# Performance work log

Hardware: AMD Instinct MI355X
Metric: run time of the kernel (lower is better)

The kernel has to match this reference:

```python
import jax, jax.numpy as jnp
import numpy as np

B, L, D, H, FF = 2, 4096, 512, 8, 2048
HD = D // H
EPS = 1e-5


def _layer_norm(x, g, b):
    mu = jnp.mean(x, axis=-1, keepdims=True)
    var = jnp.mean(jnp.square(x - mu), axis=-1, keepdims=True)
    return (x - mu) * jax.lax.rsqrt(var + EPS) * g + b


def setup_inputs() -> dict:
    key = jax.random.key(0)
    ks = jax.random.split(key, 16)
    s = 1.0 / np.sqrt(D)
    inp = {
        'x': jax.random.normal(ks[0], (B, L, D), dtype=jnp.float32),
        'Wq': jax.random.normal(ks[1], (D, D), dtype=jnp.float32) * s,
        'bq': jnp.zeros((D,), jnp.float32),
        'Wk': jax.random.normal(ks[2], (D, D), dtype=jnp.float32) * s,
        'bk': jnp.zeros((D,), jnp.float32),
        'Wv': jax.random.normal(ks[3], (D, D), dtype=jnp.float32) * s,
        'bv': jnp.zeros((D,), jnp.float32),
        'Wo': jax.random.normal(ks[4], (D, D), dtype=jnp.float32) * s,
        'bo': jnp.zeros((D,), jnp.float32),
        'ln1_g': jnp.ones((D,), jnp.float32),
        'ln1_b': jnp.zeros((D,), jnp.float32),
        'W1': jax.random.normal(ks[5], (D, FF), dtype=jnp.float32) * s,
        'b1': jnp.zeros((FF,), jnp.float32),
        'W2': jax.random.normal(ks[6], (FF, D), dtype=jnp.float32) * (1.0 / np.sqrt(FF)),
        'b2': jnp.zeros((D,), jnp.float32),
        'ln2_g': jnp.ones((D,), jnp.float32),
        'ln2_b': jnp.zeros((D,), jnp.float32),
        'window': 128,
    }
    return inp


def reference(x, Wq, bq, Wk, bk, Wv, bv, Wo, bo, ln1_g, ln1_b, W1, b1, W2, b2, ln2_g, ln2_b, window):
    # ---- local (banded) self-attention, matching nn.MultiheadAttention math ----
    q = (x @ Wq + bq).reshape(B, L, H, HD)
    k = (x @ Wk + bk).reshape(B, L, H, HD)
    v = (x @ Wv + bv).reshape(B, L, H, HD)
    scale = 1.0 / np.sqrt(HD)
    scores = jnp.einsum('bqhd,bkhd->bhqk', q, k) * scale  # [B,H,L,L]
    idx = jnp.arange(L)
    band = jnp.abs(idx[None, :] - idx[:, None]) > window   # True = masked
    scores = jnp.where(band[None, None], -jnp.inf, scores)
    probs = jax.nn.softmax(scores, axis=-1)
    attn = jnp.einsum('bhqk,bkhd->bqhd', probs, v).reshape(B, L, D)
    attn = attn @ Wo + bo
    # ---- residual + norm1 ----
    h = _layer_norm(x + attn, ln1_g, ln1_b)
    # ---- FFN + residual + norm2 (dropout=0 at eval) ----
    ff = jax.nn.relu(h @ W1 + b1) @ W2 + b2
    return _layer_norm(h + ff, ln2_g, ln2_b)
```

## Files before the change

### kernel.cpp

```cpp
#include <hip/hip_runtime.h>

namespace {

constexpr int B = 2, L = 4096, D = 512, H = 8, FF = 2048;
constexpr int M = B * L;
constexpr float LN_EPS = 1e-5f;

typedef __attribute__((ext_vector_type(8))) short short8;
typedef __attribute__((ext_vector_type(4))) float floatx4;

typedef __attribute__((address_space(3))) unsigned int lds_uint;
typedef const __attribute__((address_space(1))) unsigned int glob_uint;

__device__ __forceinline__ void gl_lds16(const unsigned short* g, unsigned short* l) {
  __builtin_amdgcn_global_load_lds((glob_uint*)g, (lds_uint*)l, 16, 0, 0);
}

__device__ __forceinline__ unsigned short f2bf(float f) {
  union { float f; unsigned u; } v; v.f = f;
  unsigned r = v.u + 0x7FFFu + ((v.u >> 16) & 1u);
  return (unsigned short)(r >> 16);
}

__device__ __forceinline__ float bf2f(unsigned short b) {
  union { unsigned u; float f; } v; v.u = ((unsigned)b) << 16;
  return v.f;
}

__global__ __launch_bounds__(256)
void k_prep(const float* __restrict__ x,
            const float* __restrict__ Wq, const float* __restrict__ Wk,
            const float* __restrict__ Wv, const float* __restrict__ Wo,
            const float* __restrict__ W1, const float* __restrict__ W2,
            const float* __restrict__ bq, const float* __restrict__ bk,
            const float* __restrict__ bv,
            unsigned short* __restrict__ Xb,
            unsigned short* __restrict__ WqkvT, unsigned short* __restrict__ WoT,
            unsigned short* __restrict__ W1T, unsigned short* __restrict__ W2T,
            float* __restrict__ bqkv) {
  __shared__ unsigned short tile[64 * 72];
  if (blockIdx.x < 4102) {
    int tid = blockIdx.x * blockDim.x + threadIdx.x;
    if (tid < 1048576) {
      float4 v = ((const float4*)x)[tid];
      ((ushort4*)Xb)[tid] = make_ushort4(f2bf(v.x), f2bf(v.y), f2bf(v.z), f2bf(v.w));
      return;
    }
    int u = tid - 1048576;
    if (u < 1536) bqkv[u] = (u < 512) ? bq[u] : (u < 1024 ? bk[u - 512] : bv[u - 1024]);
    return;
  }
  const int t = blockIdx.x - 4102;
  const float* src; unsigned short* dst; int Ns, Kd, n0, k0, nsrc0;
  if (t < 192) {
    int nt = t % 24, kt = t / 24; int ng = nt * 64;
    src = ng < 512 ? Wq : (ng < 1024 ? Wk : Wv);
    Ns = 512; Kd = 512; n0 = ng; nsrc0 = ng & 511; k0 = kt * 64; dst = WqkvT;
  } else if (t < 256) {
    int u = t - 192; int nt = u % 8, kt = u / 8;
    src = Wo; Ns = 512; Kd = 512; n0 = nt * 64; nsrc0 = n0; k0 = kt * 64; dst = WoT;
  } else if (t < 512) {
    int u = t - 256; int nt = u % 32, kt = u / 32;
    src = W1; Ns = 2048; Kd = 512; n0 = nt * 64; nsrc0 = n0; k0 = kt * 64; dst = W1T;
  } else {
    int u = t - 512; int nt = u % 8, kt = u / 8;
    src = W2; Ns = 512; Kd = 2048; n0 = nt * 64; nsrc0 = n0; k0 = kt * 64; dst = W2T;
  }
  const int tid = threadIdx.x;
  {
    int r = tid >> 2, cs = (tid & 3) * 16;
    const float4* sp = (const float4*)(src + (size_t)(k0 + r) * Ns + nsrc0 + cs);
    unsigned short* tp = &tile[r * 72 + cs];
#pragma unroll
    for (int i = 0; i < 4; ++i) {
      float4 v = sp[i];
      tp[i * 4 + 0] = f2bf(v.x); tp[i * 4 + 1] = f2bf(v.y);
      tp[i * 4 + 2] = f2bf(v.z); tp[i * 4 + 3] = f2bf(v.w);
    }
  }
  __syncthreads();
  {
    int n = tid >> 2, ks = (tid & 3) * 16;
    unsigned short buf[16];
#pragma unroll
    for (int e = 0; e < 16; ++e) buf[e] = tile[(ks + e) * 72 + n];
    unsigned short* dp = dst + (size_t)(n0 + n) * Kd + k0 + ks;
    *(short8*)dp = *(const short8*)&buf[0];
    *(short8*)(dp + 8) = *(const short8*)&buf[8];
  }
}

template <int EPI>
__global__ __launch_bounds__(256, 3)
void k_gemm(const unsigned short* __restrict__ A, const unsigned short* __restrict__ BT,
            const float* __restrict__ bias, void* __restrict__ Cout,
            unsigned short* __restrict__ Vout,
            const int klen, const int N) {
  __shared__ unsigned short lA[2][128 * 32];
  __shared__ unsigned short lB[2][128 * 32];
  const int tid = threadIdx.x;
  const int wave = tid >> 6, lane = tid & 63;
  const int quad = lane >> 4, l16 = lane & 15;
  const int m0 = blockIdx.y * 128, n0 = blockIdx.x * 128;
  const int wm = (wave >> 1) * 64, wn = (wave & 1) * 64;
  const int kbeg = blockIdx.z * klen;
  const size_t Kdim = (size_t)klen * gridDim.z;

  const floatx4 fzero = {0.f, 0.f, 0.f, 0.f};
  floatx4 acc[4][4];
#pragma unroll
  for (int i = 0; i < 4; ++i)
#pragma unroll
    for (int j = 0; j < 4; ++j) acc[i][j] = fzero;

  const int r0 = tid >> 2, o0 = (tid & 3) * 8;
  const int r1 = (256 + tid) >> 2, o1 = (tid & 3) * 8;
  const unsigned short* Ag0 = A + (size_t)(m0 + r0) * Kdim + kbeg + o0;
  const unsigned short* Ag1 = A + (size_t)(m0 + r1) * Kdim + kbeg + o1;
  const unsigned short* Bg0 = BT + (size_t)(n0 + r0) * Kdim + kbeg + o0;
  const unsigned short* Bg1 = BT + (size_t)(n0 + r1) * Kdim + kbeg + o1;

  auto stage = [&](int buf, int kt) {
    gl_lds16(Ag0 + kt, &lA[buf][wave * 512]);
    gl_lds16(Ag1 + kt, &lA[buf][(4 + wave) * 512]);
    gl_lds16(Bg0 + kt, &lB[buf][wave * 512]);
    gl_lds16(Bg1 + kt, &lB[buf][(4 + wave) * 512]);
  };

  stage(0, 0);
  __syncthreads();

  int buf = 0;
  for (int kt = 0; kt < klen; kt += 32, buf ^= 1) {
    if (kt + 32 < klen) stage(buf ^ 1, kt + 32);
    short8 af[4], bf[4];
#pragma unroll
    for (int i = 0; i < 4; ++i)
      af[i] = *(const short8*)&lA[buf][(wm + i * 16 + l16) * 32 + quad * 8];
#pragma unroll
    for (int j = 0; j < 4; ++j)
      bf[j] = *(const short8*)&lB[buf][(wn + j * 16 + l16) * 32 + quad * 8];
#pragma unroll
    for (int i = 0; i < 4; ++i)
#pragma unroll
      for (int j = 0; j < 4; ++j)
        acc[i][j] = __builtin_amdgcn_mfma_f32_16x16x32_bf16(af[i], bf[j], acc[i][j], 0, 0, 0);
    __syncthreads();
  }

  float* outf = (float*)Cout + (size_t)blockIdx.z * M * N;
  const bool vblock = (EPI == 3) && (n0 >= 1024);
#pragma unroll
  for (int j = 0; j < 4; ++j) {
    const int col = n0 + wn + j * 16 + l16;
    const float bv = (blockIdx.z == 0) ? bias[col] : 0.f;
#pragma unroll
    for (int i = 0; i < 4; ++i) {
      const int row = m0 + wm + i * 16 + quad * 4;
      if (EPI == 3 && vblock) {
        const int hh = (col - 1024) >> 6, dd = (col - 1024) & 63;
        const int bb = row >> 12, keyl = row & 4095;
        ushort4 pk = make_ushort4(f2bf(acc[i][j][0] + bv), f2bf(acc[i][j][1] + bv),
                                  f2bf(acc[i][j][2] + bv), f2bf(acc[i][j][3] + bv));
        *(ushort4*)(Vout + ((size_t)(bb * 8 + hh) * 64 + dd) * L + keyl) = pk;
      } else {
#pragma unroll
        for (int r = 0; r < 4; ++r) {
          float v = acc[i][j][r] + bv;
          if (EPI == 1) v = fmaxf(v, 0.f);
          if (EPI == 2)
            outf[(size_t)(row + r) * N + col] = v;
          else
            ((unsigned short*)Cout)[(size_t)(row + r) * N + col] = f2bf(v);
        }
      }
    }
  }
}

__global__ __launch_bounds__(256, 3)
void k_attn(const unsigned short* __restrict__ QKV, const unsigned short* __restrict__ Vg,
            unsigned short* __restrict__ attnb, const int* __restrict__ wptr) {
  const int W = wptr[0];
  __shared__ unsigned short Kt[2][4096];
  __shared__ unsigned short Vt[2][4096];
  __shared__ unsigned short Pb[4][16 * 72];
  const int tid = threadIdx.x;
  const int wave = tid >> 6, lane = tid & 63;
  const int quad = lane >> 4, l16 = lane & 15;
  const int blk = blockIdx.x;
  const int qt = blk & 63, h = (blk >> 6) & 7, b = blk >> 9;
  const int q0blk = qt * 64;
  const int q0 = q0blk + wave * 16;
  const float scale = 0.125f;

  const unsigned short* Kbase = QKV + (size_t)(b * L) * 1536 + 512 + h * 64;
  const unsigned short* Vh = Vg + (size_t)(b * 8 + h) * 64 * L;

  auto stage = [&](int buf, int jbg) {
#pragma unroll
    for (int i = 0; i < 2; ++i) {
      int c = i * 256 + tid;
      int key = jbg + (c >> 3);
      int keyc = key < 0 ? 0 : (key > L - 1 ? L - 1 : key);
      int dpart = (c & 7) ^ ((c >> 3) & 7);
      gl_lds16(Kbase + (size_t)keyc * 1536 + dpart * 8,
               &Kt[buf][(i * 256 + wave * 64) * 8]);
    }
#pragma unroll
    for (int i = 0; i < 2; ++i) {
      int c = i * 256 + tid;
      int d = c >> 3;
      int kpart = (c & 7) ^ (d & 7);
      int kb = jbg + kpart * 8;
      kb = kb < 0 ? 0 : (kb > L - 8 ? L - 8 : kb);
      gl_lds16(Vh + (size_t)d * L + kb,
               &Vt[buf][(i * 256 + wave * 64) * 8]);
    }
  };

  const unsigned short* Qp = QKV + (size_t)(b * L + q0 + l16) * 1536 + h * 64;
  short8 qf0 = *(const short8*)(Qp + quad * 8);
  short8 qf1 = *(const short8*)(Qp + 32 + quad * 8);

  const floatx4 fzero = {0.f, 0.f, 0.f, 0.f};
  floatx4 o[4];
#pragma unroll
  for (int i = 0; i < 4; ++i) o[i] = fzero;
  float lsum[4] = {0.f, 0.f, 0.f, 0.f};
  unsigned short* lp = Pb[wave];
  const int sw = l16 & 7;

  stage(0, q0blk - 128);
  __syncthreads();

  for (int it = 0; it < 5; ++it) {
    const int jbg = q0blk - 128 + it * 64;
    if (it < 4) stage((it + 1) & 1, jbg + 64);
    const unsigned short* lk = Kt[it & 1];
    const unsigned short* lv = Vt[it & 1];
    floatx4 s[4];
#pragma unroll
    for (int ct = 0; ct < 4; ++ct) {
      int key = ct * 16 + l16;
      const short8 kf0 = *(const short8*)&lk[(key * 8 + (quad ^ sw)) * 8];
      const short8 kf1 = *(const short8*)&lk[(key * 8 + ((quad + 4) ^ sw)) * 8];
      floatx4 z = fzero;
      z = __builtin_amdgcn_mfma_f32_16x16x32_bf16(qf0, kf0, z, 0, 0, 0);
      z = __builtin_amdgcn_mfma_f32_16x16x32_bf16(qf1, kf1, z, 0, 0, 0);
      s[ct] = z;
    }
#pragma unroll
    for (int r = 0; r < 4; ++r) {
      int q = q0 + quad * 4 + r;
#pragma unroll
      for (int ct = 0; ct < 4; ++ct) {
        int key = jbg + ct * 16 + l16;
        int d = q - key; d = d < 0 ? -d : d;
        bool ok = (key >= 0) && (key < L) && (d <= W);
        float p = ok ? __expf(s[ct][r] * scale) : 0.f;
        lsum[r] += p;
        lp[(quad * 4 + r) * 72 + ct * 16 + l16] = f2bf(p);
      }
    }
    short8 pf0 = *(const short8*)&lp[l16 * 72 + quad * 8];
    short8 pf1 = *(const short8*)&lp[l16 * 72 + 32 + quad * 8];
#pragma unroll
    for (int nt = 0; nt < 4; ++nt) {
      int d = nt * 16 + l16;
      const short8 vf0 = *(const short8*)&lv[(d * 8 + (quad ^ sw)) * 8];
      const short8 vf1 = *(const short8*)&lv[(d * 8 + ((quad + 4) ^ sw)) * 8];
      o[nt] = __builtin_amdgcn_mfma_f32_16x16x32_bf16(pf0, vf0, o[nt], 0, 0, 0);
      o[nt] = __builtin_amdgcn_mfma_f32_16x16x32_bf16(pf1, vf1, o[nt], 0, 0, 0);
    }
    __syncthreads();
  }
#pragma unroll
  for (int r = 0; r < 4; ++r) {
#pragma unroll
    for (int dd = 1; dd < 16; dd <<= 1) lsum[r] += __shfl_xor(lsum[r], dd, 64);
  }
#pragma unroll
  for (int r = 0; r < 4; ++r) {
    float inv = 1.f / lsum[r];
    size_t base = (size_t)(b * L + q0 + quad * 4 + r) * 512 + h * 64;
#pragma unroll
    for (int nt = 0; nt < 4; ++nt)
      attnb[base + nt * 16 + l16] = f2bf(o[nt][r] * inv);
  }
}

template <int RESBF>
__global__ __launch_bounds__(256, 2)
void k_res_ln(const float* __restrict__ t0, const float* __restrict__ t1,
              const void* __restrict__ res,
              const float* __restrict__ gamma, const float* __restrict__ beta,
              float* __restrict__ outf, unsigned short* __restrict__ outb) {
  const int wave = threadIdx.x >> 6, lane = threadIdx.x & 63;
  const int row = blockIdx.x * 4 + wave;
  const float4* tv = (const float4*)(t0 + (size_t)row * D);
  float4 a0 = tv[lane], a1 = tv[lane + 64];
  float4 b0, b1;
  if (RESBF) {
    const ushort4* rv = (const ushort4*)((const unsigned short*)res + (size_t)row * D);
    ushort4 u0 = rv[lane], u1 = rv[lane + 64];
    b0 = make_float4(bf2f(u0.x), bf2f(u0.y), bf2f(u0.z), bf2f(u0.w));
    b1 = make_float4(bf2f(u1.x), bf2f(u1.y), bf2f(u1.z), bf2f(u1.w));
  } else {
    const float4* rv = (const float4*)((const float*)res + (size_t)row * D);
    b0 = rv[lane]; b1 = rv[lane + 64];
  }
  float4 y0 = make_float4(a0.x + b0.x, a0.y + b0.y, a0.z + b0.z, a0.w + b0.w);
  float4 y1 = make_float4(a1.x + b1.x, a1.y + b1.y, a1.z + b1.z, a1.w + b1.w);
  {
    const float4* uv = (const float4*)(t1 + (size_t)row * D);
    float4 c0 = uv[lane], c1 = uv[lane + 64];
    y0.x += c0.x; y0.y += c0.y; y0.z += c0.z; y0.w += c0.w;
    y1.x += c1.x; y1.y += c1.y; y1.z += c1.z; y1.w += c1.w;
  }
  float s = y0.x + y0.y + y0.z + y0.w + y1.x + y1.y + y1.z + y1.w;
  float q = y0.x * y0.x + y0.y * y0.y + y0.z * y0.z + y0.w * y0.w +
            y1.x * y1.x + y1.y * y1.y + y1.z * y1.z + y1.w * y1.w;
#pragma unroll
  for (int d = 1; d < 64; d <<= 1) {
    s += __shfl_xor(s, d, 64);
    q += __shfl_xor(q, d, 64);
  }
  const float mean = s * (1.f / D);
  const float var = q * (1.f / D) - mean * mean;
  const float rstd = rsqrtf(var + LN_EPS);
  float4 g0 = ((const float4*)gamma)[lane], g1 = ((const float4*)gamma)[lane + 64];
  float4 e0 = ((const float4*)beta)[lane], e1 = ((const float4*)beta)[lane + 64];
  float4 o0 = make_float4((y0.x - mean) * rstd * g0.x + e0.x, (y0.y - mean) * rstd * g0.y + e0.y,
                          (y0.z - mean) * rstd * g0.z + e0.z, (y0.w - mean) * rstd * g0.w + e0.w);
  float4 o1 = make_float4((y1.x - mean) * rstd * g1.x + e1.x, (y1.y - mean) * rstd * g1.y + e1.y,
                          (y1.z - mean) * rstd * g1.z + e1.z, (y1.w - mean) * rstd * g1.w + e1.w);
  if (outf) {
    ((float4*)(outf + (size_t)row * D))[lane] = o0;
    ((float4*)(outf + (size_t)row * D))[lane + 64] = o1;
  }
  if (outb) {
    ((ushort4*)(outb + (size_t)row * D))[lane] =
        make_ushort4(f2bf(o0.x), f2bf(o0.y), f2bf(o0.z), f2bf(o0.w));
    ((ushort4*)(outb + (size_t)row * D))[lane + 64] =
        make_ushort4(f2bf(o1.x), f2bf(o1.y), f2bf(o1.z), f2bf(o1.w));
  }
}

}

extern "C" void kernel_launch(void* const* d_in, const int* in_sizes, int n_in,
                              void* d_out, int out_size, void* d_ws, size_t ws_size,
                              hipStream_t stream) {
  const float* x   = (const float*)d_in[0];
  const float* Wq  = (const float*)d_in[1];
  const float* bq  = (const float*)d_in[2];
  const float* Wk  = (const float*)d_in[3];
  const float* bk  = (const float*)d_in[4];
  const float* Wv  = (const float*)d_in[5];
  const float* bv  = (const float*)d_in[6];
  const float* Wo  = (const float*)d_in[7];
  const float* bo  = (const float*)d_in[8];
  const float* g1  = (const float*)d_in[9];
  const float* be1 = (const float*)d_in[10];
  const float* W1  = (const float*)d_in[11];
  const float* b1  = (const float*)d_in[12];
  const float* W2  = (const float*)d_in[13];
  const float* b2  = (const float*)d_in[14];
  const float* g2  = (const float*)d_in[15];
  const float* be2 = (const float*)d_in[16];
  const int* wptr  = (const int*)d_in[17];
  float* out = (float*)d_out;

  char* w = (char*)d_ws;
  size_t off = 0;
  auto take = [&](size_t bytes) -> void* {
    void* p = w + off;
    off += (bytes + 255) & ~(size_t)255;
    return p;
  };
  unsigned short* Xb    = (unsigned short*)take((size_t)M * D * 2);
  unsigned short* QKVb  = (unsigned short*)take((size_t)M * 1536 * 2);
  unsigned short* attnb = (unsigned short*)take((size_t)M * D * 2);
  unsigned short* Vg    = (unsigned short*)take((size_t)M * D * 2);
  unsigned short* WqkvT = (unsigned short*)take((size_t)1536 * 512 * 2);
  unsigned short* WoT   = (unsigned short*)take((size_t)512 * 512 * 2);
  unsigned short* W1T   = (unsigned short*)take((size_t)2048 * 512 * 2);
  unsigned short* W2T   = (unsigned short*)take((size_t)512 * 2048 * 2);
  float* bqkv           = (float*)take(1536 * 4);
  float* tbuf           = (float*)take((size_t)2 * M * D * 4);
  unsigned short* hb    = (unsigned short*)take((size_t)M * D * 2);
  unsigned short* ffb   = (unsigned short*)take((size_t)M * FF * 2);

  k_prep<<<4870, 256, 0, stream>>>(x, Wq, Wk, Wv, Wo, W1, W2, bq, bk, bv,
                                   Xb, WqkvT, WoT, W1T, W2T, bqkv);
  k_gemm<3><<<dim3(12, 64, 1), 256, 0, stream>>>(Xb, WqkvT, bqkv, QKVb, Vg, 512, 1536);
  k_attn<<<B * H * (L / 64), 256, 0, stream>>>(QKVb, Vg, attnb, wptr);
  k_gemm<2><<<dim3(4, 64, 2), 256, 0, stream>>>(attnb, WoT, bo, tbuf, nullptr, 256, 512);
  k_res_ln<0><<<M / 4, 256, 0, stream>>>(tbuf, tbuf + (size_t)M * D, x, g1, be1, nullptr, hb);
  k_gemm<1><<<dim3(16, 64, 1), 256, 0, stream>>>(hb, W1T, b1, ffb, nullptr, 512, 2048);
  k_gemm<2><<<dim3(4, 64, 2), 256, 0, stream>>>(ffb, W2T, b2, tbuf, nullptr, 1024, 512);
  k_res_ln<1><<<M / 4, 256, 0, stream>>>(tbuf, tbuf + (size_t)M * D, hb, g2, be2, out, nullptr);
}
```

Baseline: 246.6 us.

## Use 256x256-tile triple-buffered GEMM kernel for FFN up-projection

Adds a new GEMM kernel with 256x256 block tiles, 512 threads, and a three-stage LDS ring fed by direct global-to-LDS loads. Each wave computes a 128x64 sub-tile in two halves so the next stage's loads overlap with MFMA work. The first FFN matmul (relu(h@W1+b1)) now uses it instead of the 128-tile kernel, which raises operand reuse and cuts global traffic per FLOP. The cost is higher register and LDS pressure and only 256 blocks, which may leave some CUs underused.

After: 255.7 us. 3.7% more time.

```diff
diff --git a/kernel.cpp b/kernel.cpp
--- a/kernel.cpp
+++ b/kernel.cpp
@@ -173,6 +173,108 @@
           else
             ((unsigned short*)Cout)[(size_t)(row + r) * N + col] = f2bf(v);
         }
+      }
+    }
+  }
+}
+
+template <int EPI>
+__global__ __launch_bounds__(512, 2)
+void k_gemm256(const unsigned short* __restrict__ A, const unsigned short* __restrict__ BT,
+               const float* __restrict__ bias, void* __restrict__ Cout,
+               const int klen, const int N) {
+  __shared__ unsigned short lA[3][256 * 32];
+  __shared__ unsigned short lB[3][256 * 32];
+  const int tid = threadIdx.x;
+  const int wave = tid >> 6, lane = tid & 63;
+  const int quad = lane >> 4, l16 = lane & 15;
+  const int m0 = blockIdx.y * 256, n0 = blockIdx.x * 256;
+  const int wm = (wave >> 2) * 128, wn = (wave & 3) * 64;
+  const int kbeg = blockIdx.z * klen;
+  const size_t Kdim = (size_t)klen * gridDim.z;
+  const int NT = klen >> 5;
+
+  const floatx4 fzero = {0.f, 0.f, 0.f, 0.f};
+  floatx4 acc[8][4];
+#pragma unroll
+  for (int i = 0; i < 8; ++i)
+#pragma unroll
+    for (int j = 0; j < 4; ++j) acc[i][j] = fzero;
+
+  const int srow = tid >> 2, scol = (tid & 3) * 8;
+  const unsigned short* Ag = A + (size_t)(m0 + srow) * Kdim + kbeg + scol;
+  const unsigned short* Bg = BT + (size_t)(n0 + srow) * Kdim + kbeg + scol;
+  const size_t rstep = (size_t)128 * Kdim;
+  const int ldsw = (wave * 16) * 32;
+
+  auto stageA = [&](int nb, int t2, int half) {
+    gl_lds16(Ag + (size_t)half * rstep + t2 * 32, &lA[nb][half * 4096 + ldsw]);
+  };
+  auto stageB = [&](int nb, int t2, int half) {
+    gl_lds16(Bg + (size_t)half * rstep + t2 * 32, &lB[nb][half * 4096 + ldsw]);
+  };
+
+  stageA(0, 0, 0); stageA(0, 0, 1); stageB(0, 0, 0); stageB(0, 0, 1);
+  stageA(1, 1, 0); stageA(1, 1, 1); stageB(1, 1, 0); stageB(1, 1, 1);
+  asm volatile("s_waitcnt vmcnt(4)" ::: "memory");
+  __builtin_amdgcn_s_barrier();
+  __builtin_amdgcn_sched_barrier(0);
+
+  int buf = 0, nbuf = 2;
+  for (int t = 0; t < NT; ++t) {
+    const bool pf = (t + 2 < NT);
+    const unsigned short* la = lA[buf];
+    const unsigned short* lb = lB[buf];
+    short8 af[4], bf[4], ag[4];
+#pragma unroll
+    for (int i = 0; i < 4; ++i)
+      af[i] = *(const short8*)&la[(wm + i * 16 + l16) * 32 + quad * 8];
+#pragma unroll
+    for (int j = 0; j < 4; ++j)
+      bf[j] = *(const short8*)&lb[(wn + j * 16 + l16) * 32 + quad * 8];
+    if (pf) { stageA(nbuf, t + 2, 0); stageA(nbuf, t + 2, 1); }
+    __builtin_amdgcn_s_barrier();
+    __builtin_amdgcn_s_setprio(1);
+#pragma unroll
+    for (int i = 0; i < 4; ++i)
+#pragma unroll
+      for (int j = 0; j < 4; ++j)
+        acc[i][j] = __builtin_amdgcn_mfma_f32_16x16x32_bf16(af[i], bf[j], acc[i][j], 0, 0, 0);
+    __builtin_amdgcn_s_setprio(0);
+    __builtin_amdgcn_s_barrier();
+#pragma unroll
+    for (int i = 0; i < 4; ++i)
+      ag[i] = *(const short8*)&la[(wm + 64 + i * 16 + l16) * 32 + quad * 8];
+    if (pf) { stageB(nbuf, t + 2, 0); stageB(nbuf, t + 2, 1); }
+    __builtin_amdgcn_s_barrier();
+    __builtin_amdgcn_s_setprio(1);
+#pragma unroll
+    for (int i = 0; i < 4; ++i)
+#pragma unroll
+      for (int j = 0; j < 4; ++j)
+        acc[4 + i][j] = __builtin_amdgcn_mfma_f32_16x16x32_bf16(ag[i], bf[j], acc[4 + i][j], 0, 0, 0);
+    __builtin_amdgcn_s_setprio(0);
+    if (pf) asm volatile("s_waitcnt vmcnt(4)" ::: "memory");
+    else    asm volatile("s_waitcnt vmcnt(0)" ::: "memory");
+    __builtin_amdgcn_s_barrier();
+    __builtin_amdgcn_sched_barrier(0);
+    buf = (buf == 2) ? 0 : buf + 1;
+    nbuf = (nbuf == 2) ? 0 : nbuf + 1;
+  }
+
+  unsigned short* outp = (unsigned short*)Cout;
+#pragma unroll
+  for (int j = 0; j < 4; ++j) {
+    const int col = n0 + wn + j * 16 + l16;
+    const float bv = (blockIdx.z == 0) ? bias[col] : 0.f;
+#pragma unroll
+    for (int i = 0; i < 8; ++i) {
+      const int row = m0 + wm + i * 16 + quad * 4;
+#pragma unroll
+      for (int r = 0; r < 4; ++r) {
+        float v = acc[i][j][r] + bv;
+        if (EPI == 1) v = fmaxf(v, 0.f);
+        outp[(size_t)(row + r) * N + col] = f2bf(v);
       }
     }
   }
@@ -398,7 +500,7 @@
   k_attn<<<B * H * (L / 64), 256, 0, stream>>>(QKVb, Vg, attnb, wptr);
   k_gemm<2><<<dim3(4, 64, 2), 256, 0, stream>>>(attnb, WoT, bo, tbuf, nullptr, 256, 512);
   k_res_ln<0><<<M / 4, 256, 0, stream>>>(tbuf, tbuf + (size_t)M * D, x, g1, be1, nullptr, hb);
-  k_gemm<1><<<dim3(16, 64, 1), 256, 0, stream>>>(hb, W1T, b1, ffb, nullptr, 512, 2048);
+  k_gemm256<1><<<dim3(8, 32, 1), 512, 0, stream>>>(hb, W1T, b1, ffb, 512, 2048);
   k_gemm<2><<<dim3(4, 64, 2), 256, 0, stream>>>(ffb, W2T, b2, tbuf, nullptr, 1024, 512);
   k_res_ln<1><<<M / 4, 256, 0, stream>>>(tbuf, tbuf + (size_t)M * D, hb, g2, be2, out, nullptr);
 }
```

## Keep attention probabilities in registers by computing transposed QK^T scores

Applied to the files above, without the earlier changes.

The attention kernel now computes S^T (keys as rows) with swapped MFMA operands and a permuted key-row mapping, so each lane's score outputs line up directly with the A-operand layout needed for the P·V MFMA. This removes the per-wave LDS round trip for the probability tile and its shared buffer. The softmax row-sum reduction drops from 16-lane shuffles per row to two shuffles plus a broadcast. The K staging swizzle is changed to match the new access pattern, LDS offsets are precomputed, and the occupancy hint rises to 4 blocks per SM, which may increase register pressure.

Measured after the change: 246.5 us. About the same (-0.0%).

```diff
diff --git a/kernel.cpp b/kernel.cpp
--- a/kernel.cpp
+++ b/kernel.cpp
@@ -178,13 +178,12 @@
   }
 }
 
-__global__ __launch_bounds__(256, 3)
+__global__ __launch_bounds__(256, 4)
 void k_attn(const unsigned short* __restrict__ QKV, const unsigned short* __restrict__ Vg,
             unsigned short* __restrict__ attnb, const int* __restrict__ wptr) {
   const int W = wptr[0];
   __shared__ unsigned short Kt[2][4096];
   __shared__ unsigned short Vt[2][4096];
-  __shared__ unsigned short Pb[4][16 * 72];
   const int tid = threadIdx.x;
   const int wave = tid >> 6, lane = tid & 63;
   const int quad = lane >> 4, l16 = lane & 15;
@@ -201,9 +200,10 @@
 #pragma unroll
     for (int i = 0; i < 2; ++i) {
       int c = i * 256 + tid;
-      int key = jbg + (c >> 3);
+      int kr = c >> 3;
+      int key = jbg + kr;
       int keyc = key < 0 ? 0 : (key > L - 1 ? L - 1 : key);
-      int dpart = (c & 7) ^ ((c >> 3) & 7);
+      int dpart = (c & 7) ^ (kr & 7) ^ (((kr >> 3) & 3) << 1);
       gl_lds16(Kbase + (size_t)keyc * 1536 + dpart * 8,
                &Kt[buf][(i * 256 + wave * 64) * 8]);
     }
@@ -223,13 +223,28 @@
   short8 qf0 = *(const short8*)(Qp + quad * 8);
   short8 qf1 = *(const short8*)(Qp + 32 + quad * 8);
 
+  int koff[4][2];
+#pragma unroll
+  for (int tt = 0; tt < 4; ++tt) {
+    int krow = (tt >> 1) * 32 + ((l16 >> 2) << 3) + (tt & 1) * 4 + (l16 & 3);
+    int s2 = (krow & 7) ^ (((krow >> 3) & 3) << 1);
+    koff[tt][0] = (krow * 8 + (quad ^ s2)) * 8;
+    koff[tt][1] = (krow * 8 + ((quad + 4) ^ s2)) * 8;
+  }
+  int voff[4][2];
+#pragma unroll
+  for (int nt = 0; nt < 4; ++nt) {
+    int d = nt * 16 + l16;
+    voff[nt][0] = (d * 8 + (quad ^ (d & 7))) * 8;
+    voff[nt][1] = (d * 8 + ((quad + 4) ^ (d & 7))) * 8;
+  }
+
   const floatx4 fzero = {0.f, 0.f, 0.f, 0.f};
   floatx4 o[4];
 #pragma unroll
   for (int i = 0; i < 4; ++i) o[i] = fzero;
-  float lsum[4] = {0.f, 0.f, 0.f, 0.f};
-  unsigned short* lp = Pb[wave];
-  const int sw = l16 & 7;
+  float lsum = 0.f;
+  const int q = q0 + l16;
 
   stage(0, q0blk - 128);
   __syncthreads();
@@ -239,50 +254,45 @@
     if (it < 4) stage((it + 1) & 1, jbg + 64);
     const unsigned short* lk = Kt[it & 1];
     const unsigned short* lv = Vt[it & 1];
-    floatx4 s[4];
-#pragma unroll
-    for (int ct = 0; ct < 4; ++ct) {
-      int key = ct * 16 + l16;
-      const short8 kf0 = *(const short8*)&lk[(key * 8 + (quad ^ sw)) * 8];
-      const short8 kf1 = *(const short8*)&lk[(key * 8 + ((quad + 4) ^ sw)) * 8];
+    unsigned pu[8];
+#pragma unroll
+    for (int tt = 0; tt < 4; ++tt) {
+      const short8 kf0 = *(const short8*)&lk[koff[tt][0]];
+      const short8 kf1 = *(const short8*)&lk[koff[tt][1]];
       floatx4 z = fzero;
-      z = __builtin_amdgcn_mfma_f32_16x16x32_bf16(qf0, kf0, z, 0, 0, 0);
-      z = __builtin_amdgcn_mfma_f32_16x16x32_bf16(qf1, kf1, z, 0, 0, 0);
-      s[ct] = z;
-    }
-#pragma unroll
-    for (int r = 0; r < 4; ++r) {
-      int q = q0 + quad * 4 + r;
-#pragma unroll
-      for (int ct = 0; ct < 4; ++ct) {
-        int key = jbg + ct * 16 + l16;
-        int d = q - key; d = d < 0 ? -d : d;
-        bool ok = (key >= 0) && (key < L) && (d <= W);
-        float p = ok ? __expf(s[ct][r] * scale) : 0.f;
-        lsum[r] += p;
-        lp[(quad * 4 + r) * 72 + ct * 16 + l16] = f2bf(p);
+      z = __builtin_amdgcn_mfma_f32_16x16x32_bf16(kf0, qf0, z, 0, 0, 0);
+      z = __builtin_amdgcn_mfma_f32_16x16x32_bf16(kf1, qf1, z, 0, 0, 0);
+      const int kb0 = jbg + (tt >> 1) * 32 + quad * 8 + (tt & 1) * 4;
+      float pv[4];
+#pragma unroll
+      for (int r = 0; r < 4; ++r) {
+        int key = kb0 + r;
+        int dd = q - key; dd = dd < 0 ? -dd : dd;
+        bool ok = (key >= 0) && (key < L) && (dd <= W);
+        float p = ok ? __expf(z[r] * scale) : 0.f;
+        lsum += p;
+        pv[r] = p;
       }
-    }
-    short8 pf0 = *(const short8*)&lp[l16 * 72 + quad * 8];
-    short8 pf1 = *(const short8*)&lp[l16 * 72 + 32 + quad * 8];
+      pu[tt * 2 + 0] = (unsigned)f2bf(pv[0]) | ((unsigned)f2bf(pv[1]) << 16);
+      pu[tt * 2 + 1] = (unsigned)f2bf(pv[2]) | ((unsigned)f2bf(pv[3]) << 16);
+    }
+    union { unsigned u[4]; short8 v; } pa0, pa1;
+    pa0.u[0] = pu[0]; pa0.u[1] = pu[1]; pa0.u[2] = pu[2]; pa0.u[3] = pu[3];
+    pa1.u[0] = pu[4]; pa1.u[1] = pu[5]; pa1.u[2] = pu[6]; pa1.u[3] = pu[7];
 #pragma unroll
     for (int nt = 0; nt < 4; ++nt) {
-      int d = nt * 16 + l16;
-      const short8 vf0 = *(const short8*)&lv[(d * 8 + (quad ^ sw)) * 8];
-      const short8 vf1 = *(const short8*)&lv[(d * 8 + ((quad + 4) ^ sw)) * 8];
-      o[nt] = __builtin_amdgcn_mfma_f32_16x16x32_bf16(pf0, vf0, o[nt], 0, 0, 0);
-      o[nt] = __builtin_amdgcn_mfma_f32_16x16x32_bf16(pf1, vf1, o[nt], 0, 0, 0);
+      const short8 vf0 = *(const short8*)&lv[voff[nt][0]];
+      const short8 vf1 = *(const short8*)&lv[voff[nt][1]];
+      o[nt] = __builtin_amdgcn_mfma_f32_16x16x32_bf16(pa0.v, vf0, o[nt], 0, 0, 0);
+      o[nt] = __builtin_amdgcn_mfma_f32_16x16x32_bf16(pa1.v, vf1, o[nt], 0, 0, 0);
     }
     __syncthreads();
   }
+  lsum += __shfl_xor(lsum, 16, 64);
+  lsum += __shfl_xor(lsum, 32, 64);
 #pragma unroll
   for (int r = 0; r < 4; ++r) {
-#pragma unroll
-    for (int dd = 1; dd < 16; dd <<= 1) lsum[r] += __shfl_xor(lsum[r], dd, 64);
-  }
-#pragma unroll
-  for (int r = 0; r < 4; ++r) {
-    float inv = 1.f / lsum[r];
+    float inv = 1.f / __shfl(lsum, quad * 4 + r, 64);
     size_t base = (size_t)(b * L + q0 + quad * 4 + r) * 512 + h * 64;
 #pragma unroll
     for (int nt = 0; nt < 4; ++nt)
```
